# Performance work log

Measured on AMD Instinct MI355X. Metric: run time of the kernel, lower is better.

The kernel has to match this reference:

```python
import jax, jax.numpy as jnp
import numpy as np

NUM_TAGS = 128
NUM_FEATURES = 500000
B, T, F = 64, 512, 8


def setup_inputs() -> dict:
    key = jax.random.key(0)
    ks = jax.random.split(key, 6)
    feats = jax.random.randint(ks[0], (B, T, F), 0, NUM_FEATURES)
    tags = jax.random.randint(ks[1], (B, T), 0, NUM_TAGS)
    # original init: uniform(-0.01, 0.01)
    state_weights = jax.random.uniform(ks[2], (NUM_TAGS, NUM_FEATURES), minval=-0.01, maxval=0.01, dtype=jnp.float32)
    transitions = jax.random.uniform(ks[3], (NUM_TAGS, NUM_TAGS), minval=-0.01, maxval=0.01, dtype=jnp.float32)
    start_transitions = jax.random.uniform(ks[4], (NUM_TAGS,), minval=-0.01, maxval=0.01, dtype=jnp.float32)
    end_transitions = jax.random.uniform(ks[5], (NUM_TAGS,), minval=-0.01, maxval=0.01, dtype=jnp.float32)
    return dict(feats=feats, tags=tags, state_weights=state_weights,
                transitions=transitions, start_transitions=start_transitions,
                end_transitions=end_transitions)


def reference(feats, tags, state_weights, transitions, start_transitions, end_transitions):
    """Batched CRF negative log-likelihood per sentence: logZ - gold_score. Returns [B]."""
    # emissions[b,t,k] = sum_f state_weights[k, feats[b,t,f]]  (emissions_for_sentence)
    emissions = jnp.take(state_weights, feats, axis=1).sum(-1)   # [K,B,T]
    emissions = jnp.moveaxis(emissions, 0, -1)                    # [B,T,K]

    # log_partition: forward algorithm over T via scan
    alpha0 = start_transitions[None, :] + emissions[:, 0]         # [B,K]

    def step(alpha, em_t):
        # scores[b,i,j] = alpha[b,i] + transitions[i,j]
        scores = alpha[:, :, None] + transitions[None, :, :]
        return jax.nn.logsumexp(scores, axis=1) + em_t, None

    em_rest = jnp.moveaxis(emissions[:, 1:], 1, 0)                # [T-1,B,K]
    alphaT, _ = jax.lax.scan(step, alpha0, em_rest)
    log_z = jax.nn.logsumexp(alphaT + end_transitions[None, :], axis=1)   # [B]

    # gold_score, vectorized over batch
    em_gold = jnp.take_along_axis(emissions, tags[..., None], axis=2)[..., 0].sum(axis=1)  # [B]
    trans_gold = transitions[tags[:, :-1], tags[:, 1:]].sum(axis=1)                        # [B]
    gold = start_transitions[tags[:, 0]] + end_transitions[tags[:, -1]] + em_gold + trans_gold

    return log_z - gold
```

## Files before the change

### kernel.cpp

```cpp
#include <hip/hip_runtime.h>

#define NUM_TAGS 128
#define NUM_FEATS 500000
#define BB 64
#define TT 512
#define FF 8

#define SWT_BYTES 256000000ull
#define EM_BYTES  16777216ull
#define NEED_FULL (SWT_BYTES + EM_BYTES)

__global__ __launch_bounds__(256) void transpose_kernel(
    const float* __restrict__ sw, float* __restrict__ swT) {
  __shared__ float tile[32][129];
  const int f0 = blockIdx.x * 32;
  const int t = threadIdx.x;
  const int fi = t & 31, kb = t >> 5;
#pragma unroll
  for (int it = 0; it < 16; ++it) {
    int k = kb + it * 8;
    tile[fi][k] = sw[(size_t)k * NUM_FEATS + f0 + fi];
  }
  __syncthreads();
  const int k2 = t & 127, fo = t >> 7;
#pragma unroll
  for (int it = 0; it < 16; ++it) {
    int f2 = fo + it * 2;
    swT[(size_t)(f0 + f2) * NUM_TAGS + k2] = tile[f2][k2];
  }
}

__global__ __launch_bounds__(128) void gather_t_kernel(
    const int* __restrict__ feats, const float* __restrict__ swT,
    float* __restrict__ em_exp) {
  const int token = blockIdx.x;
  const int k = threadIdx.x;
  const int* f = feats + token * FF;
  float s = 0.f;
#pragma unroll
  for (int i = 0; i < FF; ++i) s += swT[(size_t)f[i] * NUM_TAGS + k];
  em_exp[(size_t)token * NUM_TAGS + k] = __expf(s);
}

__global__ __launch_bounds__(128) void gather_f_kernel(
    const int* __restrict__ feats, const float* __restrict__ sw,
    float* __restrict__ em_exp) {
  const int token = blockIdx.x;
  const int k = threadIdx.x;
  const int* f = feats + token * FF;
  const float* row = sw + (size_t)k * NUM_FEATS;
  float s = 0.f;
#pragma unroll
  for (int i = 0; i < FF; ++i) s += row[f[i]];
  em_exp[(size_t)token * NUM_TAGS + k] = __expf(s);
}

__global__ __launch_bounds__(512, 1) void fwd_kernel(
    const float* __restrict__ em_exp, const int* __restrict__ tags,
    const float* __restrict__ trans, const float* __restrict__ startT,
    const float* __restrict__ endT, float* __restrict__ out) {
  const int b = blockIdx.x;
  const int tid = threadIdx.x;
  const int q = tid >> 7, j = tid & 127;

  __shared__ __align__(16) float alpha[NUM_TAGS];
  __shared__ __align__(16) float partial[NUM_TAGS * 4];
  __shared__ float sred[16];

  float eT[32];
#pragma unroll
  for (int i = 0; i < 32; ++i)
    eT[i] = __expf(trans[(32 * q + i) * NUM_TAGS + j]);

  const float* embx = em_exp + (size_t)b * TT * NUM_TAGS;

  if (q == 0) alpha[j] = __expf(startT[j]) * embx[j];
  __syncthreads();

  float ev_next = embx[NUM_TAGS + j];
  for (int t = 1; t < TT; ++t) {
    float ev = ev_next;
    if (t + 1 < TT) ev_next = embx[(t + 1) * NUM_TAGS + j];

    const float4* a4 = (const float4*)alpha + q * 8;
    float acc = 0.f, acc2 = 0.f;
#pragma unroll
    for (int i = 0; i < 8; ++i) {
      float4 a = a4[i];
      acc  = fmaf(a.x, eT[4 * i + 0], acc);
      acc2 = fmaf(a.y, eT[4 * i + 1], acc2);
      acc  = fmaf(a.z, eT[4 * i + 2], acc);
      acc2 = fmaf(a.w, eT[4 * i + 3], acc2);
    }
    partial[j * 4 + q] = acc + acc2;
    __syncthreads();
    float4 p = *(const float4*)&partial[j * 4];
    if (q == 0) alpha[j] = (p.x + p.y + p.z + p.w) * ev * 0.0078125f;
    __syncthreads();
  }

  if (q == 0) {
    float val = alpha[j] * __expf(endT[j]);
#pragma unroll
    for (int off = 32; off > 0; off >>= 1) val += __shfl_down(val, off, 64);
    if ((j & 63) == 0) sred[j >> 6] = val;
  }

  const int* tb = tags + b * TT;
  const int t = tid;
  const int tg = tb[t];
  float g = __logf(embx[t * NUM_TAGS + tg]);
  if (t < TT - 1) g += trans[tg * NUM_TAGS + tb[t + 1]];
  if (t == 0) g += startT[tb[0]] + endT[tb[TT - 1]];
#pragma unroll
  for (int off = 32; off > 0; off >>= 1) g += __shfl_down(g, off, 64);
  if ((tid & 63) == 0) sred[8 + (tid >> 6)] = g;
  __syncthreads();

  if (tid == 0) {
    float logz = __logf(sred[0] + sred[1]) + 511.0f * 7.0f * 0.69314718055994531f;
    float gs = 0.f;
#pragma unroll
    for (int i = 0; i < 8; ++i) gs += sred[8 + i];
    out[b] = logz - gs;
  }
}

extern "C" void kernel_launch(void* const* d_in, const int* in_sizes, int n_in,
                              void* d_out, int out_size, void* d_ws, size_t ws_size,
                              hipStream_t stream) {
  const int* feats = (const int*)d_in[0];
  const int* tags = (const int*)d_in[1];
  const float* sw = (const float*)d_in[2];
  const float* trans = (const float*)d_in[3];
  const float* startT = (const float*)d_in[4];
  const float* endT = (const float*)d_in[5];
  float* out = (float*)d_out;

  if (ws_size >= NEED_FULL) {
    float* swT = (float*)d_ws;
    float* em_exp = (float*)((char*)d_ws + SWT_BYTES);
    transpose_kernel<<<NUM_FEATS / 32, 256, 0, stream>>>(sw, swT);
    gather_t_kernel<<<BB * TT, 128, 0, stream>>>(feats, swT, em_exp);
    fwd_kernel<<<BB, 512, 0, stream>>>(em_exp, tags, trans, startT, endT, out);
  } else {
    float* em_exp = (float*)d_ws;
    gather_f_kernel<<<BB * TT, 128, 0, stream>>>(feats, sw, em_exp);
    fwd_kernel<<<BB, 512, 0, stream>>>(em_exp, tags, trans, startT, endT, out);
  }
}
```

Baseline: 566.6 us.

## Use bf16 MFMA for CRF forward recursion and store transposed weights in bf16

Rewrites the forward recursion so each block handles 16 sentences and computes alpha·exp(trans) with bf16 MFMA 16x16x32 instructions, double-buffering alpha in shared memory and needing one barrier per step instead of two. The transposed state-weight buffer is stored as bf16, which halves the transpose write traffic and the gather read traffic. Only 4 blocks are now launched for the forward pass, and bf16 rounding of alpha, weights and transitions at every step adds numerical error.

```diff
diff --git a/kernel.cpp b/kernel.cpp
--- a/kernel.cpp
+++ b/kernel.cpp
@@ -6,12 +6,23 @@
 #define TT 512
 #define FF 8
 
-#define SWT_BYTES 256000000ull
+#define SWT_BYTES 128000000ull
 #define EM_BYTES  16777216ull
 #define NEED_FULL (SWT_BYTES + EM_BYTES)
 
+typedef __attribute__((ext_vector_type(8))) short short8;
+typedef __attribute__((ext_vector_type(4))) float float4v;
+
+__device__ inline unsigned short f2bf(float f) {
+  unsigned u = __float_as_uint(f);
+  return (unsigned short)((u + 0x7fffu + ((u >> 16) & 1u)) >> 16);
+}
+__device__ inline float bf2f(unsigned short h) {
+  return __uint_as_float(((unsigned)h) << 16);
+}
+
 __global__ __launch_bounds__(256) void transpose_kernel(
-    const float* __restrict__ sw, float* __restrict__ swT) {
+    const float* __restrict__ sw, unsigned short* __restrict__ swT) {
   __shared__ float tile[32][129];
   const int f0 = blockIdx.x * 32;
   const int t = threadIdx.x;
@@ -22,23 +33,25 @@
     tile[fi][k] = sw[(size_t)k * NUM_FEATS + f0 + fi];
   }
   __syncthreads();
-  const int k2 = t & 127, fo = t >> 7;
-#pragma unroll
-  for (int it = 0; it < 16; ++it) {
-    int f2 = fo + it * 2;
-    swT[(size_t)(f0 + f2) * NUM_TAGS + k2] = tile[f2][k2];
+  const int kp = (t & 63) * 2, fo = t >> 6;
+#pragma unroll
+  for (int it = 0; it < 8; ++it) {
+    int f2 = fo + it * 4;
+    unsigned v = (unsigned)f2bf(tile[f2][kp]) |
+                 ((unsigned)f2bf(tile[f2][kp + 1]) << 16);
+    *(unsigned*)&swT[(size_t)(f0 + f2) * NUM_TAGS + kp] = v;
   }
 }
 
 __global__ __launch_bounds__(128) void gather_t_kernel(
-    const int* __restrict__ feats, const float* __restrict__ swT,
+    const int* __restrict__ feats, const unsigned short* __restrict__ swT,
     float* __restrict__ em_exp) {
   const int token = blockIdx.x;
   const int k = threadIdx.x;
   const int* f = feats + token * FF;
   float s = 0.f;
 #pragma unroll
-  for (int i = 0; i < FF; ++i) s += swT[(size_t)f[i] * NUM_TAGS + k];
+  for (int i = 0; i < FF; ++i) s += bf2f(swT[(size_t)f[i] * NUM_TAGS + k]);
   em_exp[(size_t)token * NUM_TAGS + k] = __expf(s);
 }
 
@@ -55,74 +68,136 @@
   em_exp[(size_t)token * NUM_TAGS + k] = __expf(s);
 }
 
-__global__ __launch_bounds__(512, 1) void fwd_kernel(
+#define NB 16
+#define LROW 136
+#define LBUF (NB * LROW)
+
+__global__ __launch_bounds__(256, 1) void fwd_kernel(
     const float* __restrict__ em_exp, const int* __restrict__ tags,
     const float* __restrict__ trans, const float* __restrict__ startT,
     const float* __restrict__ endT, float* __restrict__ out) {
-  const int b = blockIdx.x;
+  __shared__ __align__(16) unsigned short abuf[2][LBUF];
+  __shared__ float red[16][17];
+
   const int tid = threadIdx.x;
-  const int q = tid >> 7, j = tid & 127;
-
-  __shared__ __align__(16) float alpha[NUM_TAGS];
-  __shared__ __align__(16) float partial[NUM_TAGS * 4];
-  __shared__ float sred[16];
-
-  float eT[32];
-#pragma unroll
-  for (int i = 0; i < 32; ++i)
-    eT[i] = __expf(trans[(32 * q + i) * NUM_TAGS + j]);
-
-  const float* embx = em_exp + (size_t)b * TT * NUM_TAGS;
-
-  if (q == 0) alpha[j] = __expf(startT[j]) * embx[j];
-  __syncthreads();
-
-  float ev_next = embx[NUM_TAGS + j];
+  const int bl = tid & 15;
+  const int h = (tid >> 4) & 3;
+  const int w = tid >> 6;
+  const int bg = blockIdx.x * NB + bl;
+
+  short8 afrag[2][4];
+#pragma unroll
+  for (int mt = 0; mt < 2; ++mt) {
+    const int j = (2 * w + mt) * 16 + bl;
+#pragma unroll
+    for (int kc = 0; kc < 4; ++kc) {
+      short8 a;
+#pragma unroll
+      for (int jj = 0; jj < 8; ++jj) {
+        int i = kc * 32 + h * 8 + jj;
+        a[jj] = (short)f2bf(__expf(trans[i * NUM_TAGS + j]) * 0.0078125f);
+      }
+      afrag[mt][kc] = a;
+    }
+  }
+
+  const float* emb = em_exp + (size_t)bg * TT * NUM_TAGS;
+
+  {
+    const int jc = tid >> 4, j0 = jc * 8;
+#pragma unroll
+    for (int jj = 0; jj < 8; ++jj)
+      abuf[0][bl * LROW + j0 + jj] =
+          f2bf(__expf(startT[j0 + jj]) * emb[j0 + jj]);
+  }
+  __syncthreads();
+
+  float4v ev[2];
+#pragma unroll
+  for (int mt = 0; mt < 2; ++mt) {
+    int j0 = (2 * w + mt) * 16 + h * 4;
+    ev[mt] = *(const float4v*)&emb[(size_t)NUM_TAGS + j0];
+  }
+
   for (int t = 1; t < TT; ++t) {
-    float ev = ev_next;
-    if (t + 1 < TT) ev_next = embx[(t + 1) * NUM_TAGS + j];
-
-    const float4* a4 = (const float4*)alpha + q * 8;
-    float acc = 0.f, acc2 = 0.f;
-#pragma unroll
-    for (int i = 0; i < 8; ++i) {
-      float4 a = a4[i];
-      acc  = fmaf(a.x, eT[4 * i + 0], acc);
-      acc2 = fmaf(a.y, eT[4 * i + 1], acc2);
-      acc  = fmaf(a.z, eT[4 * i + 2], acc);
-      acc2 = fmaf(a.w, eT[4 * i + 3], acc2);
-    }
-    partial[j * 4 + q] = acc + acc2;
+    const unsigned short* cur = abuf[(t - 1) & 1];
+    unsigned short* nxt = abuf[t & 1];
+
+    short8 bfrag[4];
+#pragma unroll
+    for (int kc = 0; kc < 4; ++kc)
+      bfrag[kc] = *(const short8*)&cur[bl * LROW + kc * 32 + h * 8];
+
+    float4v acc0 = {0.f, 0.f, 0.f, 0.f}, acc1 = {0.f, 0.f, 0.f, 0.f};
+#pragma unroll
+    for (int kc = 0; kc < 4; ++kc) {
+      acc0 = __builtin_amdgcn_mfma_f32_16x16x32_bf16(afrag[0][kc], bfrag[kc], acc0, 0, 0, 0);
+      acc1 = __builtin_amdgcn_mfma_f32_16x16x32_bf16(afrag[1][kc], bfrag[kc], acc1, 0, 0, 0);
+    }
+
+    float4v e0 = ev[0], e1 = ev[1];
+    if (t + 1 < TT) {
+#pragma unroll
+      for (int mt = 0; mt < 2; ++mt) {
+        int j0 = (2 * w + mt) * 16 + h * 4;
+        ev[mt] = *(const float4v*)&emb[(size_t)(t + 1) * NUM_TAGS + j0];
+      }
+    }
+    {
+      int j0 = (2 * w + 0) * 16 + h * 4;
+      uint2 u;
+      u.x = (unsigned)f2bf(acc0[0] * e0[0]) | ((unsigned)f2bf(acc0[1] * e0[1]) << 16);
+      u.y = (unsigned)f2bf(acc0[2] * e0[2]) | ((unsigned)f2bf(acc0[3] * e0[3]) << 16);
+      *(uint2*)&nxt[bl * LROW + j0] = u;
+    }
+    {
+      int j0 = (2 * w + 1) * 16 + h * 4;
+      uint2 u;
+      u.x = (unsigned)f2bf(acc1[0] * e1[0]) | ((unsigned)f2bf(acc1[1] * e1[1]) << 16);
+      u.y = (unsigned)f2bf(acc1[2] * e1[2]) | ((unsigned)f2bf(acc1[3] * e1[3]) << 16);
+      *(uint2*)&nxt[bl * LROW + j0] = u;
+    }
     __syncthreads();
-    float4 p = *(const float4*)&partial[j * 4];
-    if (q == 0) alpha[j] = (p.x + p.y + p.z + p.w) * ev * 0.0078125f;
-    __syncthreads();
-  }
-
-  if (q == 0) {
-    float val = alpha[j] * __expf(endT[j]);
-#pragma unroll
-    for (int off = 32; off > 0; off >>= 1) val += __shfl_down(val, off, 64);
-    if ((j & 63) == 0) sred[j >> 6] = val;
-  }
-
-  const int* tb = tags + b * TT;
-  const int t = tid;
-  const int tg = tb[t];
-  float g = __logf(embx[t * NUM_TAGS + tg]);
-  if (t < TT - 1) g += trans[tg * NUM_TAGS + tb[t + 1]];
-  if (t == 0) g += startT[tb[0]] + endT[tb[TT - 1]];
-#pragma unroll
-  for (int off = 32; off > 0; off >>= 1) g += __shfl_down(g, off, 64);
-  if ((tid & 63) == 0) sred[8 + (tid >> 6)] = g;
-  __syncthreads();
-
-  if (tid == 0) {
-    float logz = __logf(sred[0] + sred[1]) + 511.0f * 7.0f * 0.69314718055994531f;
-    float gs = 0.f;
-#pragma unroll
-    for (int i = 0; i < 8; ++i) gs += sred[8 + i];
-    out[b] = logz - gs;
+  }
+
+  {
+    const int jc = tid >> 4, j0 = jc * 8;
+    const unsigned short* fin = abuf[(TT - 1) & 1];
+    float val = 0.f;
+#pragma unroll
+    for (int jj = 0; jj < 8; ++jj)
+      val += bf2f(fin[bl * LROW + j0 + jj]) * __expf(endT[j0 + jj]);
+    red[jc][bl] = val;
+  }
+  __syncthreads();
+  float logzv = 0.f;
+  if (tid < 16) {
+    float s = 0.f;
+#pragma unroll
+    for (int q = 0; q < 16; ++q) s += red[q][tid];
+    logzv = __logf(s) + 511.0f * 7.0f * 0.69314718055994531f;
+  }
+  __syncthreads();
+
+  {
+    const int seg = tid >> 4;
+    const int* tb = tags + (size_t)bg * TT;
+    float g = 0.f;
+    for (int t = seg * 32; t < seg * 32 + 32; ++t) {
+      int tg = tb[t];
+      g += __logf(emb[(size_t)t * NUM_TAGS + tg]);
+      if (t < TT - 1) g += trans[tg * NUM_TAGS + tb[t + 1]];
+    }
+    if (seg == 0) g += startT[tb[0]];
+    if (seg == 15) g += endT[tb[TT - 1]];
+    red[seg][bl] = g;
+  }
+  __syncthreads();
+  if (tid < 16) {
+    float s = 0.f;
+#pragma unroll
+    for (int q = 0; q < 16; ++q) s += red[q][tid];
+    out[blockIdx.x * NB + tid] = logzv - s;
   }
 }
 
@@ -138,14 +213,14 @@
   float* out = (float*)d_out;
 
   if (ws_size >= NEED_FULL) {
-    float* swT = (float*)d_ws;
+    unsigned short* swT = (unsigned short*)d_ws;
     float* em_exp = (float*)((char*)d_ws + SWT_BYTES);
     transpose_kernel<<<NUM_FEATS / 32, 256, 0, stream>>>(sw, swT);
     gather_t_kernel<<<BB * TT, 128, 0, stream>>>(feats, swT, em_exp);
-    fwd_kernel<<<BB, 512, 0, stream>>>(em_exp, tags, trans, startT, endT, out);
+    fwd_kernel<<<BB / NB, 256, 0, stream>>>(em_exp, tags, trans, startT, endT, out);
   } else {
     float* em_exp = (float*)d_ws;
     gather_f_kernel<<<BB * TT, 128, 0, stream>>>(feats, sw, em_exp);
-    fwd_kernel<<<BB, 512, 0, stream>>>(em_exp, tags, trans, startT, endT, out);
-  }
-}
+    fwd_kernel<<<BB / NB, 256, 0, stream>>>(em_exp, tags, trans, startT, endT, out);
+  }
+}
```

After: 633.9 us. +11.9%, slower.
